# Optimization experiments

Measured on AMD Instinct MI355X. Metric: run time of the kernel, lower is better.

The kernel has to match this reference:

```python
import jax, jax.numpy as jnp
import numpy as np

# (multiplicity, irrep dim 2l+1, is_scalar) for '128x0e + 64x1o + 32x2e'
IRREPS = [(128, 1, True), (64, 3, False), (32, 5, False)]
EPS = 1e-05
NUM_GRAPHS = 64


def setup_inputs() -> dict:
    key = jax.random.key(0)
    k1, k2 = jax.random.split(key)
    N, dim = 200000, 480
    x = jax.random.normal(k1, (N, dim), dtype=jnp.float32)
    batch_id = jnp.sort(jax.random.randint(k2, (N,), 0, NUM_GRAPHS)).astype(jnp.int64)
    weight = jnp.ones((224,), dtype=jnp.float32)   # per-irrep-channel scale
    bias = jnp.zeros((128,), dtype=jnp.float32)    # scalar channels only
    return {"input": x, "batch_id_tensor": batch_id, "weight": weight, "bias": bias}


def _segment_mean(vals, seg, num_segments):
    # vals: (N, mul) -> per-graph mean (G, mul)
    sums = jax.ops.segment_sum(vals, seg, num_segments=num_segments)
    counts = jax.ops.segment_sum(jnp.ones((vals.shape[0],), vals.dtype), seg,
                                 num_segments=num_segments)
    return sums / jnp.maximum(counts, 1.0)[:, None]


def reference(input, batch_id_tensor, weight, bias):
    N = input.shape[0]
    seg = batch_id_tensor.astype(jnp.int32)
    ix = iw = ib = 0
    outs = []
    for mul, d, is_scalar in IRREPS:
        f = input[:, ix:ix + mul * d].reshape(N, mul, d)
        ix += mul * d
        if is_scalar:
            # instance norm: per-graph mean of scalar channels, gathered back
            m = _segment_mean(f[:, :, 0], seg, NUM_GRAPHS)[seg]  # (N, mul)
            f = f - m[:, :, None]
        # 'component' normalization: mean of squares over irrep dim
        fn = jnp.mean(f * f, axis=2)                             # (N, mul)
        # reduce='mean' over (trivial) spatial axis, then per-graph mean
        fn = _segment_mean(fn, seg, NUM_GRAPHS)[seg]             # (N, mul)
        fn = (fn + EPS) ** -0.5 * weight[iw:iw + mul]
        iw += mul
        f = f * fn[:, :, None]
        if is_scalar:
            f = f + bias[ib:ib + mul][:, None]
            ib += mul
        outs.append(f.reshape(N, mul * d))
    return jnp.concatenate(outs, axis=1)
```

## Files before the change

kernel.cpp:

```cpp
#include <hip/hip_runtime.h>

#define NGRAPHS 64
#define DIM 480
#define NCH 224
#define EPS 1e-5f
#define ROWS_PER_BLOCK 256

#define OFF_SUMSQ 0
#define OFF_SUM   14336
#define OFF_A     22528
#define OFF_B     53248
#define OFF_START 83968
#define NZERO     22528

__device__ __forceinline__ int col2ch(int col) {
    if (col < 128) return col;
    if (col < 320) return 128 + (col - 128) / 3;
    return 192 + (col - 320) / 5;
}

__global__ __launch_bounds__(256) void zero_kernel(float* ws) {
    int i = blockIdx.x * 256 + threadIdx.x;
    if (i < NZERO) ws[i] = 0.0f;
}

__global__ void start_kernel(const int* __restrict__ bid, int* __restrict__ start, int N) {
    int g = threadIdx.x;
    if (g > NGRAPHS) return;
    int lo = 0, hi = N;
    while (lo < hi) {
        int mid = (lo + hi) >> 1;
        if (bid[mid] < g) lo = mid + 1; else hi = mid;
    }
    start[g] = lo;
}

__device__ __forceinline__ void flush_stats(float* __restrict__ ws, int g, int tx,
                                            float (&ssq)[8], float (&ssum)[4]) {
    float* sq = ws + OFF_SUMSQ + (size_t)g * NCH;
    float* sm = ws + OFF_SUM   + (size_t)g * 128;
#pragma unroll
    for (int j = 0; j < 4; ++j) {
        int col = 4 * tx + j;
        atomicAdd(&sq[col2ch(col)], ssq[j]);
        ssq[j] = 0.0f;
        if (col < 128) { atomicAdd(&sm[col], ssum[j]); ssum[j] = 0.0f; }
    }
    if (tx < 56) {
#pragma unroll
        for (int j = 0; j < 4; ++j) {
            int col = 256 + 4 * tx + j;
            atomicAdd(&sq[col2ch(col)], ssq[4 + j]);
            ssq[4 + j] = 0.0f;
        }
    }
}

__global__ __launch_bounds__(256) void stats_kernel(const float* __restrict__ x,
                                                    const int* __restrict__ bid,
                                                    float* __restrict__ ws, int N) {
    const int tx = threadIdx.x & 63;
    const int ty = threadIdx.x >> 6;
    const int r0 = blockIdx.x * ROWS_PER_BLOCK;
    const int r1 = min(r0 + ROWS_PER_BLOCK, N);

    float ssq[8] = {0, 0, 0, 0, 0, 0, 0, 0};
    float ssum[4] = {0, 0, 0, 0};
    int gcur = -1;

    for (int r = r0 + ty; r < r1; r += 4) {
        int g = bid[r];
        if (g != gcur) {
            if (gcur >= 0) flush_stats(ws, gcur, tx, ssq, ssum);
            gcur = g;
        }
        const float4* rowp = (const float4*)(x + (size_t)r * DIM);
        float4 v0 = rowp[tx];
        ssq[0] += v0.x * v0.x; ssq[1] += v0.y * v0.y;
        ssq[2] += v0.z * v0.z; ssq[3] += v0.w * v0.w;
        if (tx < 32) {
            ssum[0] += v0.x; ssum[1] += v0.y; ssum[2] += v0.z; ssum[3] += v0.w;
        }
        if (tx < 56) {
            float4 v1 = rowp[64 + tx];
            ssq[4] += v1.x * v1.x; ssq[5] += v1.y * v1.y;
            ssq[6] += v1.z * v1.z; ssq[7] += v1.w * v1.w;
        }
    }
    if (gcur >= 0) flush_stats(ws, gcur, tx, ssq, ssum);
}

__global__ __launch_bounds__(256) void finalize_kernel(float* __restrict__ ws,
                                                       const float* __restrict__ w,
                                                       const float* __restrict__ b) {
    int idx = blockIdx.x * 256 + threadIdx.x;
    if (idx >= NGRAPHS * DIM) return;
    int g = idx / DIM;
    int col = idx % DIM;
    const int* start = (const int*)(ws + OFF_START);
    float cnt = (float)max(start[g + 1] - start[g], 1);
    int ch = col2ch(col);
    float ssq = ws[OFF_SUMSQ + (size_t)g * NCH + ch];
    float Av, Bv;
    if (col < 128) {
        float m   = ws[OFF_SUM + (size_t)g * 128 + col] / cnt;
        float var = ssq / cnt - m * m;
        float inv = 1.0f / sqrtf(var + EPS);
        Av = inv * w[ch];
        Bv = b[col] - m * Av;
    } else if (col < 320) {
        float fnm = ssq / (3.0f * cnt);
        Av = (1.0f / sqrtf(fnm + EPS)) * w[ch];
        Bv = 0.0f;
    } else {
        float fnm = ssq / (5.0f * cnt);
        Av = (1.0f / sqrtf(fnm + EPS)) * w[ch];
        Bv = 0.0f;
    }
    ws[OFF_A + idx] = Av;
    ws[OFF_B + idx] = Bv;
}

__global__ __launch_bounds__(256) void norm_kernel(const float* __restrict__ x,
                                                   const int* __restrict__ bid,
                                                   const float* __restrict__ ws,
                                                   float* __restrict__ out, int n4) {
    const float* A = ws + OFF_A;
    const float* B = ws + OFF_B;
    int stride = gridDim.x * 256;
    for (int i = blockIdx.x * 256 + threadIdx.x; i < n4; i += stride) {
        int row = i / (DIM / 4);
        int c4  = i % (DIM / 4);
        int g = bid[row];
        float4 xv = ((const float4*)x)[i];
        float4 av = *(const float4*)(A + (size_t)g * DIM + c4 * 4);
        float4 bv = *(const float4*)(B + (size_t)g * DIM + c4 * 4);
        float4 o;
        o.x = xv.x * av.x + bv.x;
        o.y = xv.y * av.y + bv.y;
        o.z = xv.z * av.z + bv.z;
        o.w = xv.w * av.w + bv.w;
        ((float4*)out)[i] = o;
    }
}

extern "C" void kernel_launch(void* const* d_in, const int* in_sizes, int n_in,
                              void* d_out, int out_size, void* d_ws, size_t ws_size,
                              hipStream_t stream) {
    const float* x   = (const float*)d_in[0];
    const int*   bid = (const int*)d_in[1];
    const float* w   = (const float*)d_in[2];
    const float* b   = (const float*)d_in[3];
    float* ws  = (float*)d_ws;
    float* out = (float*)d_out;
    const int N = in_sizes[1];

    zero_kernel<<<(NZERO + 255) / 256, 256, 0, stream>>>(ws);
    start_kernel<<<1, 128, 0, stream>>>(bid, (int*)(ws + OFF_START), N);
    stats_kernel<<<(N + ROWS_PER_BLOCK - 1) / ROWS_PER_BLOCK, 256, 0, stream>>>(x, bid, ws, N);
    finalize_kernel<<<(NGRAPHS * DIM + 255) / 256, 256, 0, stream>>>(ws, w, b);
    int n4 = N * (DIM / 4);
    norm_kernel<<<2048, 256, 0, stream>>>(x, bid, ws, out, n4);
}
```

Baseline: 310.4 us.

## Tile rows per graph, fuse finalize into norm, reduce stats in shared memory

```diff
diff --git a/kernel.cpp b/kernel.cpp
--- a/kernel.cpp
+++ b/kernel.cpp
@@ -4,14 +4,15 @@
 #define DIM 480
 #define NCH 224
 #define EPS 1e-5f
-#define ROWS_PER_BLOCK 256
-
-#define OFF_SUMSQ 0
+#define TILE 128
+
+typedef float f32x4 __attribute__((ext_vector_type(4)));
+
+#define OFF_SSQ   0
 #define OFF_SUM   14336
-#define OFF_A     22528
-#define OFF_B     53248
-#define OFF_START 83968
-#define NZERO     22528
+#define OFF_START 22528
+#define OFF_TPRE  22593
+#define ZN_FLOATS 22528
 
 __device__ __forceinline__ int col2ch(int col) {
     if (col < 128) return col;
@@ -19,61 +20,77 @@
     return 192 + (col - 320) / 5;
 }
 
-__global__ __launch_bounds__(256) void zero_kernel(float* ws) {
-    int i = blockIdx.x * 256 + threadIdx.x;
-    if (i < NZERO) ws[i] = 0.0f;
-}
-
-__global__ void start_kernel(const int* __restrict__ bid, int* __restrict__ start, int N) {
+__global__ __launch_bounds__(256) void init_kernel(const int* __restrict__ bid,
+                                                   float* __restrict__ ws, int N) {
+    int b = blockIdx.x;
+    if (b < 88) {
+        int i = b * 256 + threadIdx.x;
+        if (i < ZN_FLOATS) ws[i] = 0.0f;
+        return;
+    }
+    int* start = (int*)(ws + OFF_START);
+    int* tpre  = (int*)(ws + OFF_TPRE);
     int g = threadIdx.x;
-    if (g > NGRAPHS) return;
-    int lo = 0, hi = N;
-    while (lo < hi) {
+    if (g <= NGRAPHS) {
+        int lo = 0, hi = N;
+        while (lo < hi) {
+            int mid = (lo + hi) >> 1;
+            if (bid[mid] < g) lo = mid + 1; else hi = mid;
+        }
+        start[g] = lo;
+    }
+    __syncthreads();
+    if (threadIdx.x == 0) {
+        int acc = 0;
+        for (int gg = 0; gg < NGRAPHS; ++gg) {
+            tpre[gg] = acc;
+            int cnt = start[gg + 1] - start[gg];
+            acc += (cnt + TILE - 1) / TILE;
+        }
+        tpre[NGRAPHS] = acc;
+    }
+}
+
+__device__ __forceinline__ void block_tile(const int* __restrict__ tpre, int b,
+                                           int& g, int& tile) {
+    int lo = 0, hi = NGRAPHS;
+    while (hi - lo > 1) {
         int mid = (lo + hi) >> 1;
-        if (bid[mid] < g) lo = mid + 1; else hi = mid;
-    }
-    start[g] = lo;
-}
-
-__device__ __forceinline__ void flush_stats(float* __restrict__ ws, int g, int tx,
-                                            float (&ssq)[8], float (&ssum)[4]) {
-    float* sq = ws + OFF_SUMSQ + (size_t)g * NCH;
-    float* sm = ws + OFF_SUM   + (size_t)g * 128;
-#pragma unroll
-    for (int j = 0; j < 4; ++j) {
-        int col = 4 * tx + j;
-        atomicAdd(&sq[col2ch(col)], ssq[j]);
-        ssq[j] = 0.0f;
-        if (col < 128) { atomicAdd(&sm[col], ssum[j]); ssum[j] = 0.0f; }
-    }
-    if (tx < 56) {
-#pragma unroll
-        for (int j = 0; j < 4; ++j) {
-            int col = 256 + 4 * tx + j;
-            atomicAdd(&sq[col2ch(col)], ssq[4 + j]);
-            ssq[4 + j] = 0.0f;
-        }
-    }
+        if (tpre[mid] <= b) lo = mid; else hi = mid;
+    }
+    g = lo;
+    tile = b - tpre[lo];
+}
+
+__device__ __forceinline__ void flush_quad(float* __restrict__ SQ, int col0,
+                                           float v0, float v1, float v2, float v3) {
+    float v[4] = {v0, v1, v2, v3};
+    int ch0 = col2ch(col0), ch1 = col2ch(col0 + 1),
+        ch2 = col2ch(col0 + 2), ch3 = col2ch(col0 + 3);
+    float acc = v[0]; int cur = ch0;
+    if (ch1 == cur) acc += v[1]; else { atomicAdd(&SQ[cur], acc); cur = ch1; acc = v[1]; }
+    if (ch2 == cur) acc += v[2]; else { atomicAdd(&SQ[cur], acc); cur = ch2; acc = v[2]; }
+    if (ch3 == cur) acc += v[3]; else { atomicAdd(&SQ[cur], acc); cur = ch3; acc = v[3]; }
+    atomicAdd(&SQ[cur], acc);
 }
 
 __global__ __launch_bounds__(256) void stats_kernel(const float* __restrict__ x,
-                                                    const int* __restrict__ bid,
-                                                    float* __restrict__ ws, int N) {
+                                                    float* __restrict__ ws) {
+    const int* start = (const int*)(ws + OFF_START);
+    const int* tpre  = (const int*)(ws + OFF_TPRE);
+    if ((int)blockIdx.x >= tpre[NGRAPHS]) return;
+    int g, tile;
+    block_tile(tpre, blockIdx.x, g, tile);
+    int r0 = start[g] + tile * TILE;
+    int r1 = min(r0 + TILE, start[g + 1]);
+
     const int tx = threadIdx.x & 63;
     const int ty = threadIdx.x >> 6;
-    const int r0 = blockIdx.x * ROWS_PER_BLOCK;
-    const int r1 = min(r0 + ROWS_PER_BLOCK, N);
 
     float ssq[8] = {0, 0, 0, 0, 0, 0, 0, 0};
     float ssum[4] = {0, 0, 0, 0};
-    int gcur = -1;
 
     for (int r = r0 + ty; r < r1; r += 4) {
-        int g = bid[r];
-        if (g != gcur) {
-            if (gcur >= 0) flush_stats(ws, gcur, tx, ssq, ssum);
-            gcur = g;
-        }
         const float4* rowp = (const float4*)(x + (size_t)r * DIM);
         float4 v0 = rowp[tx];
         ssq[0] += v0.x * v0.x; ssq[1] += v0.y * v0.y;
@@ -87,60 +104,91 @@
             ssq[6] += v1.z * v1.z; ssq[7] += v1.w * v1.w;
         }
     }
-    if (gcur >= 0) flush_stats(ws, gcur, tx, ssq, ssum);
-}
-
-__global__ __launch_bounds__(256) void finalize_kernel(float* __restrict__ ws,
-                                                       const float* __restrict__ w,
-                                                       const float* __restrict__ b) {
-    int idx = blockIdx.x * 256 + threadIdx.x;
-    if (idx >= NGRAPHS * DIM) return;
-    int g = idx / DIM;
-    int col = idx % DIM;
+
+    __shared__ float red[256][12];
+#pragma unroll
+    for (int j = 0; j < 8; ++j) red[threadIdx.x][j] = ssq[j];
+#pragma unroll
+    for (int j = 0; j < 4; ++j) red[threadIdx.x][8 + j] = ssum[j];
+    __syncthreads();
+
+    if (ty == 0) {
+        float s[8], sm[4];
+#pragma unroll
+        for (int j = 0; j < 8; ++j)
+            s[j] = red[tx][j] + red[tx + 64][j] + red[tx + 128][j] + red[tx + 192][j];
+#pragma unroll
+        for (int j = 0; j < 4; ++j)
+            sm[j] = red[tx][8 + j] + red[tx + 64][8 + j] + red[tx + 128][8 + j] + red[tx + 192][8 + j];
+
+        float* SQ = ws + OFF_SSQ + (size_t)g * NCH;
+        float* SM = ws + OFF_SUM + (size_t)g * 128;
+        flush_quad(SQ, 4 * tx, s[0], s[1], s[2], s[3]);
+        if (tx < 32) {
+#pragma unroll
+            for (int j = 0; j < 4; ++j) atomicAdd(&SM[4 * tx + j], sm[j]);
+        }
+        if (tx < 56) flush_quad(SQ, 256 + 4 * tx, s[4], s[5], s[6], s[7]);
+    }
+}
+
+__global__ __launch_bounds__(256) void norm_kernel(const float* __restrict__ x,
+                                                   const float* __restrict__ w,
+                                                   const float* __restrict__ bias,
+                                                   const float* __restrict__ ws,
+                                                   float* __restrict__ out) {
     const int* start = (const int*)(ws + OFF_START);
+    const int* tpre  = (const int*)(ws + OFF_TPRE);
+    int total = tpre[NGRAPHS];
+    int b = total - 1 - (int)blockIdx.x;
+    if (b < 0) return;
+    int t = threadIdx.x;
+    if (t >= 240) return;
+    int g, tile;
+    block_tile(tpre, b, g, tile);
+    int r0 = start[g] + tile * TILE;
+    int r1 = min(r0 + TILE, start[g + 1]);
+
+    int row_off = t / 120;
+    int c4 = t - row_off * 120;
+
     float cnt = (float)max(start[g + 1] - start[g], 1);
-    int ch = col2ch(col);
-    float ssq = ws[OFF_SUMSQ + (size_t)g * NCH + ch];
-    float Av, Bv;
-    if (col < 128) {
-        float m   = ws[OFF_SUM + (size_t)g * 128 + col] / cnt;
-        float var = ssq / cnt - m * m;
-        float inv = 1.0f / sqrtf(var + EPS);
-        Av = inv * w[ch];
-        Bv = b[col] - m * Av;
-    } else if (col < 320) {
-        float fnm = ssq / (3.0f * cnt);
-        Av = (1.0f / sqrtf(fnm + EPS)) * w[ch];
-        Bv = 0.0f;
-    } else {
-        float fnm = ssq / (5.0f * cnt);
-        Av = (1.0f / sqrtf(fnm + EPS)) * w[ch];
-        Bv = 0.0f;
-    }
-    ws[OFF_A + idx] = Av;
-    ws[OFF_B + idx] = Bv;
-}
-
-__global__ __launch_bounds__(256) void norm_kernel(const float* __restrict__ x,
-                                                   const int* __restrict__ bid,
-                                                   const float* __restrict__ ws,
-                                                   float* __restrict__ out, int n4) {
-    const float* A = ws + OFF_A;
-    const float* B = ws + OFF_B;
-    int stride = gridDim.x * 256;
-    for (int i = blockIdx.x * 256 + threadIdx.x; i < n4; i += stride) {
-        int row = i / (DIM / 4);
-        int c4  = i % (DIM / 4);
-        int g = bid[row];
-        float4 xv = ((const float4*)x)[i];
-        float4 av = *(const float4*)(A + (size_t)g * DIM + c4 * 4);
-        float4 bv = *(const float4*)(B + (size_t)g * DIM + c4 * 4);
-        float4 o;
-        o.x = xv.x * av.x + bv.x;
-        o.y = xv.y * av.y + bv.y;
-        o.z = xv.z * av.z + bv.z;
-        o.w = xv.w * av.w + bv.w;
-        ((float4*)out)[i] = o;
+    const float* SQ = ws + OFF_SSQ + (size_t)g * NCH;
+    const float* SM = ws + OFF_SUM + (size_t)g * 128;
+
+    float A[4], B[4];
+#pragma unroll
+    for (int j = 0; j < 4; ++j) {
+        int col = 4 * c4 + j;
+        int ch = col2ch(col);
+        float ssq = SQ[ch];
+        if (col < 128) {
+            float m   = SM[col] / cnt;
+            float var = ssq / cnt - m * m;
+            float Av  = rsqrtf(var + EPS) * w[ch];
+            A[j] = Av;
+            B[j] = bias[col] - m * Av;
+        } else {
+            float d = (col < 320) ? 3.0f : 5.0f;
+            A[j] = rsqrtf(ssq / (d * cnt) + EPS) * w[ch];
+            B[j] = 0.0f;
+        }
+    }
+
+    const float4* xp = (const float4*)(x + (size_t)(r0 + row_off) * DIM) + c4;
+    float*        op = out + (size_t)(r0 + row_off) * DIM + 4 * c4;
+    const int stride4 = 2 * (DIM / 4);
+    const int strideF = 2 * DIM;
+    for (int r = r0 + row_off; r < r1; r += 2) {
+        float4 xv = *xp;
+        f32x4 o;
+        o.x = xv.x * A[0] + B[0];
+        o.y = xv.y * A[1] + B[1];
+        o.z = xv.z * A[2] + B[2];
+        o.w = xv.w * A[3] + B[3];
+        __builtin_nontemporal_store(o, (f32x4*)op);
+        xp += stride4;
+        op += strideF;
     }
 }
 
@@ -155,10 +203,9 @@
     float* out = (float*)d_out;
     const int N = in_sizes[1];
 
-    zero_kernel<<<(NZERO + 255) / 256, 256, 0, stream>>>(ws);
-    start_kernel<<<1, 128, 0, stream>>>(bid, (int*)(ws + OFF_START), N);
-    stats_kernel<<<(N + ROWS_PER_BLOCK - 1) / ROWS_PER_BLOCK, 256, 0, stream>>>(x, bid, ws, N);
-    finalize_kernel<<<(NGRAPHS * DIM + 255) / 256, 256, 0, stream>>>(ws, w, b);
-    int n4 = N * (DIM / 4);
-    norm_kernel<<<2048, 256, 0, stream>>>(x, bid, ws, out, n4);
-}
+    int max_tiles = (N + TILE - 1) / TILE + NGRAPHS;
+
+    init_kernel<<<89, 256, 0, stream>>>(bid, ws, N);
+    stats_kernel<<<max_tiles, 256, 0, stream>>>(x, ws);
+    norm_kernel<<<max_tiles, 256, 0, stream>>>(x, w, b, ws, out);
+}
```

After: 257.1 us. 17.2% less time.
